# Performance work log

Measured on AMD Instinct MI355X. Metric: run time of the kernel, lower is better.

Reference implementation:

```python
import jax, jax.numpy as jnp
import numpy as np

N_HEAD, D_K, D_MODEL = 8, 64, 512  # factorized_k == d_k == d_v forced by view()/einsum consistency
B, LQ, LK = 4, 2048, 2048
TEMP = float(np.sqrt(D_K))
NEG = -1000000000.0


def setup_inputs() -> dict:
    key = jax.random.key(0)
    ks = jax.random.split(key, 8)
    q = jax.random.normal(ks[0], (B, LQ, D_MODEL), jnp.float32)
    k = jax.random.normal(ks[1], (B, LK, D_MODEL), jnp.float32)
    v = jax.random.normal(ks[2], (B, LK, D_MODEL), jnp.float32)
    mask = jax.random.randint(ks[3], (B, LQ, LK), 0, 2).astype(jnp.int32)
    # torch.rand-style positive uniform params, scaled to keep the 4-matmul chain O(1)
    W_A = jax.random.uniform(ks[4], (D_MODEL, D_K), jnp.float32, 0.0, 1.0 / D_K)
    W_A2 = jax.random.uniform(ks[5], (D_MODEL, D_K), jnp.float32, 0.0, 1.0 / D_K)
    W_A3 = jax.random.uniform(ks[6], (D_MODEL, D_K), jnp.float32, 0.0, 1.0 / D_K)
    fc_w = jax.random.normal(ks[7], (D_MODEL, N_HEAD * D_K), jnp.float32) / np.float32(np.sqrt(N_HEAD * D_K))
    ln_gamma = jnp.ones((D_MODEL,), jnp.float32)
    ln_beta = jnp.zeros((D_MODEL,), jnp.float32)
    return dict(q=q, k=k, v=v, mask=mask, W_A=W_A, W_A2=W_A2, W_A3=W_A3,
                fc_w=fc_w, ln_gamma=ln_gamma, ln_beta=ln_beta)


def reference(q, k, v, mask, W_A, W_A2, W_A3, fc_w, ln_gamma, ln_beta):
    b, lq, dm = q.shape
    lk = k.shape[1]
    residual = q
    # Since factorized_k == d_k, view(n_head,d_k,-1) and view(n_head,-1,d_k) coincide.
    W_a = W_A.reshape(N_HEAD, D_K, D_K)    # plays both 'bcd' (W_A) and 'bdi' (W_B)
    W_a2 = W_A2.reshape(N_HEAD, D_K, D_K)  # plays both 'bim' (W_At) and 'bmj' (W_Bt)
    W_av = W_A3.reshape(N_HEAD, D_K, D_K)  # plays both 'bna' (W_av) and 'bac' (W_bv)

    kt = jnp.swapaxes(k, 1, 2).reshape(b, N_HEAD, D_K, lk)  # [b,h,dk,lk]
    qh = q.reshape(b, lq, N_HEAD, D_K)                       # [b,lq,h,dk]
    vh = v.reshape(b, lk, N_HEAD, D_K)                       # [b,lk,h,dk]

    # Fold the tiny per-head weight chain first (same math as the 6-tensor einsum).
    Wq = jnp.einsum('hcd,hdi,him,hmj->hcj', W_a, W_a, W_a2, W_a2)  # [h,dk,dk]
    attn = jnp.einsum('kahc,hcj,khjn->khan', qh, Wq, kt) / TEMP     # [b,h,lq,lk]
    attn = jnp.where(mask[:, None, :, :] != 0, attn, NEG)
    attn = jax.nn.softmax(attn, axis=-1)  # dropout is identity in eval

    Wv = jnp.einsum('hna,hac->hnc', W_av, W_av)                    # [h,dk,dk]
    out = jnp.einsum('khjm,kmhn,hnc->khjc', attn, vh, Wv)          # [b,h,lq,dk]
    out = jnp.swapaxes(out, 1, 2).reshape(b, lq, N_HEAD * D_K)
    out = out @ fc_w.T  # Linear bias=False; dropout identity
    out = out + residual
    mu = jnp.mean(out, axis=-1, keepdims=True)
    var = jnp.mean((out - mu) ** 2, axis=-1, keepdims=True)
    out = (out - mu) / jnp.sqrt(var + 1e-6) * ln_gamma + ln_beta
    return (out, attn)
```

## Files before the change

### kernel.cpp

```cpp
#include <hip/hip_runtime.h>

#define B_ 4
#define H_ 8
#define L_ 2048
#define DM 512
#define DK 64

typedef __bf16 bf16x8 __attribute__((ext_vector_type(8)));
typedef float f32x4 __attribute__((ext_vector_type(4)));

__device__ __forceinline__ f32x4 mfma16(bf16x8 a, bf16x8 b, f32x4 c) {
  return __builtin_amdgcn_mfma_f32_16x16x32_bf16(a, b, c, 0, 0, 0);
}
__device__ __forceinline__ unsigned short f2bf(float f) {
  unsigned int u = __float_as_uint(f);
  u += 0x7fffu + ((u >> 16) & 1u);
  return (unsigned short)(u >> 16);
}
__device__ __forceinline__ void async16(const void* g, void* l) {
  __builtin_amdgcn_global_load_lds((const __attribute__((address_space(1))) unsigned int*)g,
                                   (__attribute__((address_space(3))) unsigned int*)l, 16, 0, 0);
}
__device__ __forceinline__ float rsum16(float v) {
  v += __shfl_xor(v, 1);
  v += __shfl_xor(v, 2);
  v += __shfl_xor(v, 4);
  v += __shfl_xor(v, 8);
  return v;
}

__device__ __forceinline__ void mm64(const float* X, const float* Y, float acc[4][4], int tr, int tc) {
#pragma unroll
  for (int rr = 0; rr < 4; ++rr)
#pragma unroll
    for (int cc = 0; cc < 4; ++cc) acc[rr][cc] = 0.f;
  for (int c = 0; c < 64; ++c) {
    float a0 = X[(tr + 0) * 65 + c], a1 = X[(tr + 1) * 65 + c];
    float a2 = X[(tr + 2) * 65 + c], a3 = X[(tr + 3) * 65 + c];
    float b0 = Y[c * 65 + tc + 0], b1 = Y[c * 65 + tc + 1];
    float b2 = Y[c * 65 + tc + 2], b3 = Y[c * 65 + tc + 3];
    acc[0][0] += a0 * b0; acc[0][1] += a0 * b1; acc[0][2] += a0 * b2; acc[0][3] += a0 * b3;
    acc[1][0] += a1 * b0; acc[1][1] += a1 * b1; acc[1][2] += a1 * b2; acc[1][3] += a1 * b3;
    acc[2][0] += a2 * b0; acc[2][1] += a2 * b1; acc[2][2] += a2 * b2; acc[2][3] += a2 * b3;
    acc[3][0] += a3 * b0; acc[3][1] += a3 * b1; acc[3][2] += a3 * b2; acc[3][3] += a3 * b3;
  }
}

__global__ __launch_bounds__(256) void k_weights(const float* __restrict__ WA, const float* __restrict__ WA2,
                                                 const float* __restrict__ WA3, float* __restrict__ Wq,
                                                 float* __restrict__ Wv) {
  __shared__ float sA[64 * 65], sB[64 * 65], sT[64 * 65];
  const int h = blockIdx.x, t = threadIdx.x;
  const int tr = (t >> 4) * 4, tc = (t & 15) * 4;
  for (int i = t; i < 4096; i += 256) {
    int r = i >> 6, c = i & 63;
    sA[r * 65 + c] = WA[h * 4096 + i];
    sB[r * 65 + c] = WA2[h * 4096 + i];
  }
  __syncthreads();
  float acc[4][4];
  mm64(sA, sA, acc, tr, tc);
#pragma unroll
  for (int rr = 0; rr < 4; ++rr)
#pragma unroll
    for (int cc = 0; cc < 4; ++cc) sT[(tr + rr) * 65 + tc + cc] = acc[rr][cc];
  __syncthreads();
  mm64(sT, sB, acc, tr, tc);
#pragma unroll
  for (int rr = 0; rr < 4; ++rr)
#pragma unroll
    for (int cc = 0; cc < 4; ++cc) sA[(tr + rr) * 65 + tc + cc] = acc[rr][cc];
  __syncthreads();
  mm64(sA, sB, acc, tr, tc);
#pragma unroll
  for (int rr = 0; rr < 4; ++rr)
#pragma unroll
    for (int cc = 0; cc < 4; ++cc) Wq[h * 4096 + (tr + rr) * 64 + tc + cc] = acc[rr][cc];
  for (int i = t; i < 4096; i += 256) {
    int r = i >> 6, c = i & 63;
    sT[r * 65 + c] = WA3[h * 4096 + i];
  }
  __syncthreads();
  mm64(sT, sT, acc, tr, tc);
#pragma unroll
  for (int rr = 0; rr < 4; ++rr)
#pragma unroll
    for (int cc = 0; cc < 4; ++cc) Wv[h * 4096 + (tr + rr) * 64 + tc + cc] = acc[rr][cc];
}

__global__ void k_conv(const float* __restrict__ s, unsigned short* __restrict__ d, int n4) {
  int i = blockIdx.x * blockDim.x + threadIdx.x;
  int stride = gridDim.x * blockDim.x;
  for (; i < n4; i += stride) {
    float4 f = ((const float4*)s)[i];
    ushort4 o;
    o.x = f2bf(f.x); o.y = f2bf(f.y); o.z = f2bf(f.z); o.w = f2bf(f.w);
    ((ushort4*)d)[i] = o;
  }
}

__global__ __launch_bounds__(256) void k_maskpack(const int* __restrict__ mask,
                                                  unsigned long long* __restrict__ mp) {
  const int row = blockIdx.x * 4 + (threadIdx.x >> 6);
  const int lane = threadIdx.x & 63;
  const int* src = mask + (size_t)row * L_;
#pragma unroll
  for (int c = 0; c < 32; ++c) {
    int mv = src[c * 64 + lane];
    unsigned long long bits = __ballot(mv != 0);
    if (lane == 0) mp[(size_t)row * 32 + c] = bits;
  }
}

__global__ __launch_bounds__(256) void k_qprime(const float* __restrict__ q, const float* __restrict__ Wq,
                                                unsigned short* __restrict__ Qp) {
  __shared__ float sW[64 * 65], sQ[64 * 65];
  const int bid = blockIdx.x;
  const int rt = bid & 31, h = (bid >> 5) & 7, b = bid >> 8;
  const int t = threadIdx.x;
  const int row0 = rt * 64;
  const float QS = 0.125f * 1.44269504088896f;
  for (int i = t; i < 4096; i += 256) {
    int r = i >> 6, c = i & 63;
    sW[r * 65 + c] = Wq[h * 4096 + i];
    sQ[r * 65 + c] = q[(size_t)(b * L_ + row0 + r) * DM + h * DK + c];
  }
  __syncthreads();
  float acc[4][4];
  const int tr = (t >> 4) * 4, tc = (t & 15) * 4;
  mm64(sQ, sW, acc, tr, tc);
#pragma unroll
  for (int rr = 0; rr < 4; ++rr) {
    ushort4 o;
    o.x = f2bf(acc[rr][0] * QS); o.y = f2bf(acc[rr][1] * QS);
    o.z = f2bf(acc[rr][2] * QS); o.w = f2bf(acc[rr][3] * QS);
    *(ushort4*)&Qp[(size_t)(b * L_ + row0 + tr + rr) * DM + h * DK + tc] = o;
  }
}

__global__ __launch_bounds__(256) void k_vprime(const float* __restrict__ v, const float* __restrict__ Wv,
                                                unsigned short* __restrict__ VpT) {
  __shared__ float sW[64 * 65], sV[64 * 65];
  __shared__ __align__(16) unsigned short ldsT[64 * 72];
  const int bid = blockIdx.x;
  const int rt = bid & 31, h = (bid >> 5) & 7, b = bid >> 8;
  const int t = threadIdx.x;
  const int key0 = rt * 64;
  for (int i = t; i < 4096; i += 256) {
    int r = i >> 6, c = i & 63;
    sW[r * 65 + c] = Wv[h * 4096 + i];
    sV[r * 65 + c] = v[(size_t)(b * L_ + key0 + r) * DM + h * DK + c];
  }
  __syncthreads();
  float acc[4][4];
  const int tr = (t >> 4) * 4, tc = (t & 15) * 4;
  mm64(sV, sW, acc, tr, tc);
#pragma unroll
  for (int rr = 0; rr < 4; ++rr)
#pragma unroll
    for (int cc = 0; cc < 4; ++cc) ldsT[(tc + cc) * 72 + tr + rr] = f2bf(acc[rr][cc]);
  __syncthreads();
  const int dk = t >> 2, kc = t & 3;
  const uint4* srcp = (const uint4*)&ldsT[dk * 72 + kc * 16];
  uint4 v0 = srcp[0], v1 = srcp[1];
  size_t go = ((size_t)((b * H_ + h) * DK + dk)) * L_ + key0 + kc * 16;
  *(uint4*)&VpT[go] = v0;
  *(uint4*)&VpT[go + 8] = v1;
}

__global__ __launch_bounds__(256) void k_attn(const unsigned short* __restrict__ Qp,
                                              const unsigned short* __restrict__ Kb,
                                              const unsigned short* __restrict__ VpT,
                                              const unsigned long long* __restrict__ mp,
                                              float* __restrict__ attn,
                                              float* __restrict__ ov) {
  __shared__ __align__(16) unsigned short KT[2][4096];
  __shared__ __align__(16) unsigned short VT[2][4096];
  __shared__ __align__(16) unsigned short PB[4][16 * 76];
  const int bid0 = blockIdx.x;
  const int bid = (bid0 & 7) * 128 + (bid0 >> 3);
  const int qt = bid & 31;
  const int h = (bid >> 5) & 7;
  const int b = bid >> 8;
  const int tid = threadIdx.x;
  const int lane = tid & 63;
  const int w = tid >> 6;
  const int l15 = lane & 15, l4 = lane >> 4;
  const int row0 = qt * 64 + w * 16;

  const unsigned short* qb = Qp + ((size_t)(b * L_ + row0 + l15)) * DM + h * DK + l4 * 8;
  const bf16x8 aQ0 = *(const bf16x8*)qb;
  const bf16x8 aQ1 = *(const bf16x8*)(qb + 32);

  const size_t kb_base = (size_t)b * L_ * DM + h * DK;
  const size_t vt_base = (size_t)((b * H_ + h) * DK) * L_;
  const unsigned long long* mrow = mp + (size_t)(b * L_ + row0 + l4 * 4) * 32;

  const int p_lo = tid * 16;
  const int skey = p_lo >> 7;
  const int sboff = (p_lo & 127) ^ ((skey & 7) << 4);
  const int skey1 = (p_lo + 4096) >> 7;
  const int sboff1 = ((p_lo + 4096) & 127) ^ ((skey1 & 7) << 4);

#define STAGE_K(kt_, s_)                                                                   \
  {                                                                                        \
    async16(Kb + kb_base + (size_t)((kt_) * 64 + skey) * DM + (sboff >> 1),                \
            (char*)&KT[s_][0] + p_lo);                                                     \
    async16(Kb + kb_base + (size_t)((kt_) * 64 + skey1) * DM + (sboff1 >> 1),              \
            (char*)&KT[s_][0] + p_lo + 4096);                                              \
  }
#define STAGE_V(kt_, s_)                                                                   \
  {                                                                                        \
    async16(VpT + vt_base + (size_t)skey * L_ + (kt_) * 64 + (sboff >> 1),                 \
            (char*)&VT[s_][0] + p_lo);                                                     \
    async16(VpT + vt_base + (size_t)skey1 * L_ + (kt_) * 64 + (sboff1 >> 1),               \
            (char*)&VT[s_][0] + p_lo + 4096);                                              \
  }

  unsigned long long mwA[4], mwB[4];
  float lsum[4] = {0.f, 0.f, 0.f, 0.f};

#pragma unroll
  for (int r = 0; r < 4; ++r) { mwA[r] = mrow[r * 32 + 0]; mwB[r] = mrow[r * 32 + 1]; }
  STAGE_K(0, 0);
  asm volatile("s_waitcnt vmcnt(0)" ::: "memory");
  __builtin_amdgcn_s_barrier();

#define P1_BODY(KT_, VMN_, DO_STAGE_, DO_LOADM_)                                           \
  {                                                                                        \
    const int kt = (KT_);                                                                  \
    const int cur = kt & 1;                                                                \
    __builtin_amdgcn_sched_barrier(0);                                                     \
    unsigned long long mwN[4] = {0ull, 0ull, 0ull, 0ull};                                  \
    if (DO_LOADM_) {                                                                       \
      _Pragma("unroll") for (int r = 0; r < 4; ++r) mwN[r] = mrow[r * 32 + kt + 2];        \
    }                                                                                      \
    if (DO_STAGE_) STAGE_K(kt + 1, cur ^ 1);                                               \
    asm volatile("s_waitcnt vmcnt(" #VMN_ ")" ::: "memory");                               \
    __builtin_amdgcn_sched_barrier(0);                                                     \
    __builtin_amdgcn_s_barrier();                                                          \
    const char* Kbase = (const char*)&KT[cur][0];                                          \
    _Pragma("unroll") for (int f = 0; f < 4; ++f) {                                        \
      int keyrow = f * 16 + l15;                                                           \
      int sw = (keyrow & 7) << 4;                                                          \
      bf16x8 b0 = *(const bf16x8*)(Kbase + keyrow * 128 + ((l4 * 16) ^ sw));               \
      bf16x8 b1 = *(const bf16x8*)(Kbase + keyrow * 128 + ((64 + l4 * 16) ^ sw));          \
      f32x4 acc = {0.f, 0.f, 0.f, 0.f};                                                    \
      acc = mfma16(aQ0, b0, acc);                                                          \
      acc = mfma16(aQ1, b1, acc);                                                          \
      _Pragma("unroll") for (int r = 0; r < 4; ++r) {                                      \
        unsigned int hb = (unsigned int)(mwA[r] >> (f * 16));                              \
        lsum[r] += ((hb >> l15) & 1u) ? exp2f(acc[r]) : 0.f;                               \
      }                                                                                    \
    }                                                                                      \
    __builtin_amdgcn_s_barrier();                                                          \
    _Pragma("unroll") for (int r = 0; r < 4; ++r) { mwA[r] = mwB[r]; mwB[r] = mwN[r]; }    \
  }

  for (int t = 0; t < 30; ++t) P1_BODY(t, 6, true, true);
  P1_BODY(30, 2, true, false);
  P1_BODY(31, 0, false, false);
#undef P1_BODY

  float invl[4];
#pragma unroll
  for (int r = 0; r < 4; ++r) invl[r] = 1.0f / rsum16(lsum[r]);

  f32x4 O[4];
#pragma unroll
  for (int d = 0; d < 4; ++d) { f32x4 z = {0.f, 0.f, 0.f, 0.f}; O[d] = z; }

  float* arow0 = attn + ((size_t)((b * H_ + h) * L_) + row0 + l4 * 4) * L_;

#pragma unroll
  for (int r = 0; r < 4; ++r) { mwA[r] = mrow[r * 32 + 0]; mwB[r] = mrow[r * 32 + 1]; }
  STAGE_K(0, 0);
  STAGE_V(0, 0);
  asm volatile("s_waitcnt vmcnt(0)" ::: "memory");
  __builtin_amdgcn_s_barrier();

#define P2_BODY(KT_, VMN_, DO_STAGE_, DO_LOADM_)                                           \
  {                                                                                        \
    const int kt = (KT_);                                                                  \
    const int cur = kt & 1;                                                                \
    const int key0 = kt * 64;                                                              \
    __builtin_amdgcn_sched_barrier(0);                                                     \
    unsigned long long mwN[4] = {0ull, 0ull, 0ull, 0ull};                                  \
    if (DO_LOADM_) {                                                                       \
      _Pragma("unroll") for (int r = 0; r < 4; ++r) mwN[r] = mrow[r * 32 + kt + 2];        \
    }                                                                                      \
    if (DO_STAGE_) { STAGE_K(kt + 1, cur ^ 1); STAGE_V(kt + 1, cur ^ 1); }                 \
    asm volatile("s_waitcnt vmcnt(" #VMN_ ")" ::: "memory");                               \
    __builtin_amdgcn_sched_barrier(0);                                                     \
    __builtin_amdgcn_s_barrier();                                                          \
    const char* Kbase = (const char*)&KT[cur][0];                                          \
    const char* Vbase = (const char*)&VT[cur][0];                                          \
    float pvv[4][4];                                                                       \
    _Pragma("unroll") for (int f = 0; f < 4; ++f) {                                        \
      int keyrow = f * 16 + l15;                                                           \
      int sw = (keyrow & 7) << 4;                                                          \
      bf16x8 b0 = *(const bf16x8*)(Kbase + keyrow * 128 + ((l4 * 16) ^ sw));               \
      bf16x8 b1 = *(const bf16x8*)(Kbase + keyrow * 128 + ((64 + l4 * 16) ^ sw));          \
      f32x4 acc = {0.f, 0.f, 0.f, 0.f};                                                    \
      acc = mfma16(aQ0, b0, acc);                                                          \
      acc = mfma16(aQ1, b1, acc);                                                          \
      _Pragma("unroll") for (int r = 0; r < 4; ++r) {                                      \
        unsigned int hb = (unsigned int)(mwA[r] >> (f * 16));                              \
        pvv[f][r] = ((hb >> l15) & 1u) ? exp2f(acc[r]) * invl[r] : 0.f;                    \
      }                                                                                    \
    }                                                                                      \
    _Pragma("unroll") for (int f = 0; f < 4; ++f)                                          \
      _Pragma("unroll") for (int r = 0; r < 4; ++r)                                        \
        __builtin_nontemporal_store(pvv[f][r],                                             \
            arow0 + (size_t)r * L_ + key0 + f * 16 + l15);                                 \
    _Pragma("unroll") for (int f = 0; f < 4; ++f)                                          \
      _Pragma("unroll") for (int r = 0; r < 4; ++r)                                        \
        PB[w][(l4 * 4 + r) * 76 + f * 16 + l15] = f2bf(pvv[f][r]);                         \
    bf16x8 aP0 = *(const bf16x8*)((const char*)&PB[w][0] + l15 * 152 + l4 * 16);           \
    bf16x8 aP1 = *(const bf16x8*)((const char*)&PB[w][0] + l15 * 152 + 64 + l4 * 16);      \
    __builtin_amdgcn_s_setprio(1);                                                         \
    _Pragma("unroll") for (int d = 0; d < 4; ++d) {                                        \
      int dkrow = d * 16 + l15;                                                            \
      int sw = (dkrow & 7) << 4;                                                           \
      bf16x8 v0 = *(const bf16x8*)(Vbase + dkrow * 128 + ((l4 * 16) ^ sw));                \
      bf16x8 v1 = *(const bf16x8*)(Vbase + dkrow * 128 + ((64 + l4 * 16) ^ sw));           \
      O[d] = mfma16(aP0, v0, O[d]);                                                        \
      O[d] = mfma16(aP1, v1, O[d]);                                                        \
    }                                                                                      \
    __builtin_amdgcn_s_setprio(0);                                                         \
    __builtin_amdgcn_s_barrier();                                                          \
    _Pragma("unroll") for (int r = 0; r < 4; ++r) { mwA[r] = mwB[r]; mwB[r] = mwN[r]; }    \
  }

  for (int t = 0; t < 30; ++t) P2_BODY(t, 24, true, true);
  P2_BODY(30, 20, true, false);
  P2_BODY(31, 16, false, false);
#undef P2_BODY

#pragma unroll
  for (int d = 0; d < 4; ++d)
#pragma unroll
    for (int r = 0; r < 4; ++r)
      ov[(size_t)(b * L_ + row0 + l4 * 4 + r) * DM + h * DK + d * 16 + l15] = O[d][r];
#undef STAGE_K
#undef STAGE_V
}

__global__ __launch_bounds__(256) void k_proj(const float* __restrict__ qres,
                                              const unsigned short* __restrict__ fcb,
                                              const float* __restrict__ gamma,
                                              const float* __restrict__ beta,
                                              float* __restrict__ io) {
  __shared__ float red1[16][4], red2[16][4];
  const int blk = blockIdx.x;
  const int tid = threadIdx.x, lane = tid & 63, w = tid >> 6;
  const int l15 = lane & 15, l4 = lane >> 4;
  const int row0 = blk * 16;
  const float* arow = io + (size_t)(row0 + l15) * DM + l4 * 8;
  const unsigned short* bb = fcb + (size_t)(w * 128 + l15) * DM + l4 * 8;
  f32x4 C[8];
#pragma unroll
  for (int i = 0; i < 8; ++i) { f32x4 z = {0.f, 0.f, 0.f, 0.f}; C[i] = z; }
  for (int kc = 0; kc < 16; ++kc) {
    float4 a0 = *(const float4*)(arow + kc * 32);
    float4 a1 = *(const float4*)(arow + kc * 32 + 4);
    union { unsigned short u[8]; bf16x8 v; } t;
    t.u[0] = f2bf(a0.x); t.u[1] = f2bf(a0.y); t.u[2] = f2bf(a0.z); t.u[3] = f2bf(a0.w);
    t.u[4] = f2bf(a1.x); t.u[5] = f2bf(a1.y); t.u[6] = f2bf(a1.z); t.u[7] = f2bf(a1.w);
#pragma unroll
    for (int cf = 0; cf < 8; ++cf) {
      bf16x8 bv = *(const bf16x8*)(bb + (size_t)(cf * 16) * DM + kc * 32);
      C[cf] = mfma16(t.v, bv, C[cf]);
    }
  }
  float s1[4] = {0.f, 0.f, 0.f, 0.f}, s2[4] = {0.f, 0.f, 0.f, 0.f};
  const int colb = w * 128;
#pragma unroll
  for (int cf = 0; cf < 8; ++cf)
#pragma unroll
    for (int r = 0; r < 4; ++r) {
      float val = C[cf][r] + qres[(size_t)(row0 + l4 * 4 + r) * DM + colb + cf * 16 + l15];
      C[cf][r] = val;
      s1[r] += val;
      s2[r] += val * val;
    }
#pragma unroll
  for (int r = 0; r < 4; ++r) { s1[r] = rsum16(s1[r]); s2[r] = rsum16(s2[r]); }
  if (l15 == 0) {
#pragma unroll
    for (int r = 0; r < 4; ++r) { red1[l4 * 4 + r][w] = s1[r]; red2[l4 * 4 + r][w] = s2[r]; }
  }
  __syncthreads();
  float mu[4], rs[4];
#pragma unroll
  for (int r = 0; r < 4; ++r) {
    int row = l4 * 4 + r;
    float t1 = red1[row][0] + red1[row][1] + red1[row][2] + red1[row][3];
    float t2 = red2[row][0] + red2[row][1] + red2[row][2] + red2[row][3];
    float m_ = t1 * (1.0f / 512.0f);
    float var = t2 * (1.0f / 512.0f) - m_ * m_;
    mu[r] = m_;
    rs[r] = rsqrtf(var + 1e-6f);
  }
#pragma unroll
  for (int cf = 0; cf < 8; ++cf) {
    float g = gamma[colb + cf * 16 + l15];
    float be = beta[colb + cf * 16 + l15];
#pragma unroll
    for (int r = 0; r < 4; ++r)
      io[(size_t)(row0 + l4 * 4 + r) * DM + colb + cf * 16 + l15] =
          (C[cf][r] - mu[r]) * rs[r] * g + be;
  }
}

extern "C" void kernel_launch(void* const* d_in, const int* in_sizes, int n_in,
                              void* d_out, int out_size, void* d_ws, size_t ws_size,
                              hipStream_t stream) {
  (void)in_sizes; (void)n_in; (void)out_size; (void)ws_size;
  const float* q   = (const float*)d_in[0];
  const float* k   = (const float*)d_in[1];
  const float* v   = (const float*)d_in[2];
  const int* mask  = (const int*)d_in[3];
  const float* WA  = (const float*)d_in[4];
  const float* WA2 = (const float*)d_in[5];
  const float* WA3 = (const float*)d_in[6];
  const float* fcw = (const float*)d_in[7];
  const float* gam = (const float*)d_in[8];
  const float* bet = (const float*)d_in[9];
  float* out = (float*)d_out;
  float* attn = out + (size_t)B_ * L_ * DM;

  char* ws = (char*)d_ws;
  float* Wq = (float*)ws;
  float* Wv = (float*)(ws + 131072);
  unsigned short* Qp  = (unsigned short*)(ws + 262144);
  unsigned short* Kb  = (unsigned short*)(ws + 262144 + 8388608);
  unsigned short* VpT = (unsigned short*)(ws + 262144 + 2 * 8388608);
  unsigned short* FCb = (unsigned short*)(ws + 262144 + 3 * 8388608);
  unsigned long long* mp = (unsigned long long*)(ws + 262144 + 3 * 8388608 + 524288);

  k_weights<<<8, 256, 0, stream>>>(WA, WA2, WA3, Wq, Wv);
  k_conv<<<1024, 256, 0, stream>>>(k, Kb, (B_ * L_ * DM) / 4);
  k_conv<<<256, 256, 0, stream>>>(fcw, FCb, (DM * DM) / 4);
  k_maskpack<<<2048, 256, 0, stream>>>(mask, mp);
  k_qprime<<<1024, 256, 0, stream>>>(q, Wq, Qp);
  k_vprime<<<1024, 256, 0, stream>>>(v, Wv, VpT);
  k_attn<<<1024, 256, 0, stream>>>(Qp, Kb, VpT, mp, attn, out);
  k_proj<<<512, 256, 0, stream>>>(q, FCb, gam, bet, out);
}
```

Baseline: 330.2 us.

## Load K fragments directly to registers in pass 1 and swizzle P buffer

The first softmax-normalizer pass now loads K MFMA fragments straight from global memory into registers with a two-deep software pipeline, instead of staging through LDS with barriers. The change also swaps exp2f for raw v_exp_f32, replaces the padded P buffer with an XOR-swizzled 128-byte row layout, and adds an occupancy hint of 4 blocks per SM. The aim is to remove LDS staging and barrier overhead in pass 1 and cut LDS bank conflicts. The cost is higher register pressure and uncoalesced global loads in pass 1, which rely on L2 hits.

New measurement: 347.6 us. +5.3%, slower.

```diff
diff --git a/kernel.cpp b/kernel.cpp
--- a/kernel.cpp
+++ b/kernel.cpp
@@ -16,6 +16,11 @@
   unsigned int u = __float_as_uint(f);
   u += 0x7fffu + ((u >> 16) & 1u);
   return (unsigned short)(u >> 16);
+}
+__device__ __forceinline__ float fexp2(float x) {
+  float r;
+  asm("v_exp_f32 %0, %1" : "=v"(r) : "v"(x));
+  return r;
 }
 __device__ __forceinline__ void async16(const void* g, void* l) {
   __builtin_amdgcn_global_load_lds((const __attribute__((address_space(1))) unsigned int*)g,
@@ -168,15 +173,15 @@
   *(uint4*)&VpT[go + 8] = v1;
 }
 
-__global__ __launch_bounds__(256) void k_attn(const unsigned short* __restrict__ Qp,
-                                              const unsigned short* __restrict__ Kb,
-                                              const unsigned short* __restrict__ VpT,
-                                              const unsigned long long* __restrict__ mp,
-                                              float* __restrict__ attn,
-                                              float* __restrict__ ov) {
+__global__ __launch_bounds__(256, 4) void k_attn(const unsigned short* __restrict__ Qp,
+                                                 const unsigned short* __restrict__ Kb,
+                                                 const unsigned short* __restrict__ VpT,
+                                                 const unsigned long long* __restrict__ mp,
+                                                 float* __restrict__ attn,
+                                                 float* __restrict__ ov) {
   __shared__ __align__(16) unsigned short KT[2][4096];
   __shared__ __align__(16) unsigned short VT[2][4096];
-  __shared__ __align__(16) unsigned short PB[4][16 * 76];
+  __shared__ __align__(16) unsigned short PB[4][1024];
   const int bid0 = blockIdx.x;
   const int bid = (bid0 & 7) * 128 + (bid0 >> 3);
   const int qt = bid & 31;
@@ -195,6 +200,62 @@
   const size_t kb_base = (size_t)b * L_ * DM + h * DK;
   const size_t vt_base = (size_t)((b * H_ + h) * DK) * L_;
   const unsigned long long* mrow = mp + (size_t)(b * L_ + row0 + l4 * 4) * 32;
+  const unsigned short* kfrag = Kb + kb_base + (size_t)l15 * DM + l4 * 8;
+
+  float lsum[4] = {0.f, 0.f, 0.f, 0.f};
+
+  bf16x8 curF[8], nxtF[8];
+  unsigned long long mwA[4], mwN[4];
+
+#define LOADK_P1(FR, kt_)                                                                  \
+  {                                                                                        \
+    _Pragma("unroll") for (int f = 0; f < 4; ++f) {                                        \
+      const unsigned short* kp = kfrag + (size_t)((kt_) * 64 + f * 16) * DM;               \
+      FR[2 * f] = *(const bf16x8*)kp;                                                      \
+      FR[2 * f + 1] = *(const bf16x8*)(kp + 32);                                           \
+    }                                                                                      \
+  }
+#define LOADM_P1(MW, kt_)                                                                  \
+  { _Pragma("unroll") for (int r = 0; r < 4; ++r) MW[r] = mrow[r * 32 + (kt_)]; }
+#define COMP_P1(FR, MW)                                                                    \
+  {                                                                                        \
+    _Pragma("unroll") for (int f = 0; f < 4; ++f) {                                        \
+      f32x4 acc = {0.f, 0.f, 0.f, 0.f};                                                    \
+      acc = mfma16(aQ0, FR[2 * f], acc);                                                   \
+      acc = mfma16(aQ1, FR[2 * f + 1], acc);                                               \
+      _Pragma("unroll") for (int r = 0; r < 4; ++r) {                                      \
+        unsigned int hb = (unsigned int)(MW[r] >> (f * 16));                               \
+        lsum[r] += ((hb >> l15) & 1u) ? fexp2(acc[r]) : 0.f;                               \
+      }                                                                                    \
+    }                                                                                      \
+  }
+
+  LOADK_P1(curF, 0);
+  LOADM_P1(mwA, 0);
+  for (int kt2 = 0; kt2 < 16; ++kt2) {
+    const int kt = kt2 * 2;
+    LOADK_P1(nxtF, kt + 1);
+    LOADM_P1(mwN, kt + 1);
+    COMP_P1(curF, mwA);
+    if (kt2 < 15) {
+      LOADK_P1(curF, kt + 2);
+      LOADM_P1(mwA, kt + 2);
+    }
+    COMP_P1(nxtF, mwN);
+  }
+#undef LOADK_P1
+#undef LOADM_P1
+#undef COMP_P1
+
+  float invl[4];
+#pragma unroll
+  for (int r = 0; r < 4; ++r) invl[r] = 1.0f / rsum16(lsum[r]);
+
+  f32x4 O[4];
+#pragma unroll
+  for (int d = 0; d < 4; ++d) { f32x4 z = {0.f, 0.f, 0.f, 0.f}; O[d] = z; }
+
+  float* arow0 = attn + ((size_t)((b * H_ + h) * L_) + row0 + l4 * 4) * L_;
 
   const int p_lo = tid * 16;
   const int skey = p_lo >> 7;
@@ -217,67 +278,15 @@
             (char*)&VT[s_][0] + p_lo + 4096);                                              \
   }
 
-  unsigned long long mwA[4], mwB[4];
-  float lsum[4] = {0.f, 0.f, 0.f, 0.f};
-
-#pragma unroll
-  for (int r = 0; r < 4; ++r) { mwA[r] = mrow[r * 32 + 0]; mwB[r] = mrow[r * 32 + 1]; }
-  STAGE_K(0, 0);
-  asm volatile("s_waitcnt vmcnt(0)" ::: "memory");
-  __builtin_amdgcn_s_barrier();
-
-#define P1_BODY(KT_, VMN_, DO_STAGE_, DO_LOADM_)                                           \
-  {                                                                                        \
-    const int kt = (KT_);                                                                  \
-    const int cur = kt & 1;                                                                \
-    __builtin_amdgcn_sched_barrier(0);                                                     \
-    unsigned long long mwN[4] = {0ull, 0ull, 0ull, 0ull};                                  \
-    if (DO_LOADM_) {                                                                       \
-      _Pragma("unroll") for (int r = 0; r < 4; ++r) mwN[r] = mrow[r * 32 + kt + 2];        \
-    }                                                                                      \
-    if (DO_STAGE_) STAGE_K(kt + 1, cur ^ 1);                                               \
-    asm volatile("s_waitcnt vmcnt(" #VMN_ ")" ::: "memory");                               \
-    __builtin_amdgcn_sched_barrier(0);                                                     \
-    __builtin_amdgcn_s_barrier();                                                          \
-    const char* Kbase = (const char*)&KT[cur][0];                                          \
-    _Pragma("unroll") for (int f = 0; f < 4; ++f) {                                        \
-      int keyrow = f * 16 + l15;                                                           \
-      int sw = (keyrow & 7) << 4;                                                          \
-      bf16x8 b0 = *(const bf16x8*)(Kbase + keyrow * 128 + ((l4 * 16) ^ sw));               \
-      bf16x8 b1 = *(const bf16x8*)(Kbase + keyrow * 128 + ((64 + l4 * 16) ^ sw));          \
-      f32x4 acc = {0.f, 0.f, 0.f, 0.f};                                                    \
-      acc = mfma16(aQ0, b0, acc);                                                          \
-      acc = mfma16(aQ1, b1, acc);                                                          \
-      _Pragma("unroll") for (int r = 0; r < 4; ++r) {                                      \
-        unsigned int hb = (unsigned int)(mwA[r] >> (f * 16));                              \
-        lsum[r] += ((hb >> l15) & 1u) ? exp2f(acc[r]) : 0.f;                               \
-      }                                                                                    \
-    }                                                                                      \
-    __builtin_amdgcn_s_barrier();                                                          \
-    _Pragma("unroll") for (int r = 0; r < 4; ++r) { mwA[r] = mwB[r]; mwB[r] = mwN[r]; }    \
-  }
-
-  for (int t = 0; t < 30; ++t) P1_BODY(t, 6, true, true);
-  P1_BODY(30, 2, true, false);
-  P1_BODY(31, 0, false, false);
-#undef P1_BODY
-
-  float invl[4];
-#pragma unroll
-  for (int r = 0; r < 4; ++r) invl[r] = 1.0f / rsum16(lsum[r]);
-
-  f32x4 O[4];
-#pragma unroll
-  for (int d = 0; d < 4; ++d) { f32x4 z = {0.f, 0.f, 0.f, 0.f}; O[d] = z; }
-
-  float* arow0 = attn + ((size_t)((b * H_ + h) * L_) + row0 + l4 * 4) * L_;
-
+  unsigned long long mwB[4];
 #pragma unroll
   for (int r = 0; r < 4; ++r) { mwA[r] = mrow[r * 32 + 0]; mwB[r] = mrow[r * 32 + 1]; }
   STAGE_K(0, 0);
   STAGE_V(0, 0);
   asm volatile("s_waitcnt vmcnt(0)" ::: "memory");
   __builtin_amdgcn_s_barrier();
+
+  char* pbw = (char*)&PB[w][0];
 
 #define P2_BODY(KT_, VMN_, DO_STAGE_, DO_LOADM_)                                           \
   {                                                                                        \
@@ -285,9 +294,9 @@
     const int cur = kt & 1;                                                                \
     const int key0 = kt * 64;                                                              \
     __builtin_amdgcn_sched_barrier(0);                                                     \
-    unsigned long long mwN[4] = {0ull, 0ull, 0ull, 0ull};                                  \
+    unsigned long long mwN2[4] = {0ull, 0ull, 0ull, 0ull};                                 \
     if (DO_LOADM_) {                                                                       \
-      _Pragma("unroll") for (int r = 0; r < 4; ++r) mwN[r] = mrow[r * 32 + kt + 2];        \
+      _Pragma("unroll") for (int r = 0; r < 4; ++r) mwN2[r] = mrow[r * 32 + kt + 2];       \
     }                                                                                      \
     if (DO_STAGE_) { STAGE_K(kt + 1, cur ^ 1); STAGE_V(kt + 1, cur ^ 1); }                 \
     asm volatile("s_waitcnt vmcnt(" #VMN_ ")" ::: "memory");                               \
@@ -306,7 +315,7 @@
       acc = mfma16(aQ1, b1, acc);                                                          \
       _Pragma("unroll") for (int r = 0; r < 4; ++r) {                                      \
         unsigned int hb = (unsigned int)(mwA[r] >> (f * 16));                              \
-        pvv[f][r] = ((hb >> l15) & 1u) ? exp2f(acc[r]) * invl[r] : 0.f;                    \
+        pvv[f][r] = ((hb >> l15) & 1u) ? fexp2(acc[r]) * invl[r] : 0.f;                    \
       }                                                                                    \
     }                                                                                      \
     _Pragma("unroll") for (int f = 0; f < 4; ++f)                                          \
@@ -314,10 +323,14 @@
         __builtin_nontemporal_store(pvv[f][r],                                             \
             arow0 + (size_t)r * L_ + key0 + f * 16 + l15);                                 \
     _Pragma("unroll") for (int f = 0; f < 4; ++f)                                          \
-      _Pragma("unroll") for (int r = 0; r < 4; ++r)                                        \
-        PB[w][(l4 * 4 + r) * 76 + f * 16 + l15] = f2bf(pvv[f][r]);                         \
-    bf16x8 aP0 = *(const bf16x8*)((const char*)&PB[w][0] + l15 * 152 + l4 * 16);           \
-    bf16x8 aP1 = *(const bf16x8*)((const char*)&PB[w][0] + l15 * 152 + 64 + l4 * 16);      \
+      _Pragma("unroll") for (int r = 0; r < 4; ++r) {                                      \
+        int prow = l4 * 4 + r;                                                             \
+        *(unsigned short*)(pbw + prow * 128 +                                              \
+                           ((f * 32 + l15 * 2) ^ ((prow & 7) << 4))) = f2bf(pvv[f][r]);    \
+      }                                                                                    \
+    int psw = (l15 & 7) << 4;                                                              \
+    bf16x8 aP0 = *(const bf16x8*)(pbw + l15 * 128 + ((l4 * 16) ^ psw));                    \
+    bf16x8 aP1 = *(const bf16x8*)(pbw + l15 * 128 + ((64 + l4 * 16) ^ psw));               \
     __builtin_amdgcn_s_setprio(1);                                                         \
     _Pragma("unroll") for (int d = 0; d < 4; ++d) {                                        \
       int dkrow = d * 16 + l15;                                                            \
@@ -329,7 +342,7 @@
     }                                                                                      \
     __builtin_amdgcn_s_setprio(0);                                                         \
     __builtin_amdgcn_s_barrier();                                                          \
-    _Pragma("unroll") for (int r = 0; r < 4; ++r) { mwA[r] = mwB[r]; mwB[r] = mwN[r]; }    \
+    _Pragma("unroll") for (int r = 0; r < 4; ++r) { mwA[r] = mwB[r]; mwB[r] = mwN2[r]; }   \
   }
 
   for (int t = 0; t < 30; ++t) P2_BODY(t, 24, true, true);
```

## Transpose QK^T MFMA so each lane owns a query row, vectorizing attn stores

Applied to the files above, without the earlier changes.

Swaps the MFMA operand order so each lane holds four consecutive keys of a single query row instead of four rows. This reduces per-lane mask state to one 64-bit word, turns the row-sum into two cross-lane shuffles, and lets attention probabilities be written as 16-byte nontemporal vector stores instead of scalar stores. The P buffer in LDS gets a swizzled 128-byte-row layout with packed 8-byte writes. Other changes: a raw v_exp_f32 replaces exp2f, vmcnt waits are adjusted to the new load counts, and launch bounds request 4 blocks per CU. The raw exp drops denormal handling, and the extra occupancy constraint may cause register spills.

After: 319.5 us. 1.03x faster.

```diff
diff --git a/kernel.cpp b/kernel.cpp
--- a/kernel.cpp
+++ b/kernel.cpp
@@ -16,6 +16,11 @@
   unsigned int u = __float_as_uint(f);
   u += 0x7fffu + ((u >> 16) & 1u);
   return (unsigned short)(u >> 16);
+}
+__device__ __forceinline__ float fexp2(float x) {
+  float r;
+  asm("v_exp_f32 %0, %1" : "=v"(r) : "v"(x));
+  return r;
 }
 __device__ __forceinline__ void async16(const void* g, void* l) {
   __builtin_amdgcn_global_load_lds((const __attribute__((address_space(1))) unsigned int*)g,
@@ -168,15 +173,15 @@
   *(uint4*)&VpT[go + 8] = v1;
 }
 
-__global__ __launch_bounds__(256) void k_attn(const unsigned short* __restrict__ Qp,
-                                              const unsigned short* __restrict__ Kb,
-                                              const unsigned short* __restrict__ VpT,
-                                              const unsigned long long* __restrict__ mp,
-                                              float* __restrict__ attn,
-                                              float* __restrict__ ov) {
+__global__ __launch_bounds__(256, 4) void k_attn(const unsigned short* __restrict__ Qp,
+                                                 const unsigned short* __restrict__ Kb,
+                                                 const unsigned short* __restrict__ VpT,
+                                                 const unsigned long long* __restrict__ mp,
+                                                 float* __restrict__ attn,
+                                                 float* __restrict__ ov) {
   __shared__ __align__(16) unsigned short KT[2][4096];
   __shared__ __align__(16) unsigned short VT[2][4096];
-  __shared__ __align__(16) unsigned short PB[4][16 * 76];
+  __shared__ __align__(16) unsigned short PB[4][1024];
   const int bid0 = blockIdx.x;
   const int bid = (bid0 & 7) * 128 + (bid0 >> 3);
   const int qt = bid & 31;
@@ -194,7 +199,7 @@
 
   const size_t kb_base = (size_t)b * L_ * DM + h * DK;
   const size_t vt_base = (size_t)((b * H_ + h) * DK) * L_;
-  const unsigned long long* mrow = mp + (size_t)(b * L_ + row0 + l4 * 4) * 32;
+  const unsigned long long* mrowl = mp + (size_t)(b * L_ + row0 + l15) * 32;
 
   const int p_lo = tid * 16;
   const int skey = p_lo >> 7;
@@ -217,11 +222,11 @@
             (char*)&VT[s_][0] + p_lo + 4096);                                              \
   }
 
-  unsigned long long mwA[4], mwB[4];
-  float lsum[4] = {0.f, 0.f, 0.f, 0.f};
-
-#pragma unroll
-  for (int r = 0; r < 4; ++r) { mwA[r] = mrow[r * 32 + 0]; mwB[r] = mrow[r * 32 + 1]; }
+  float lsum = 0.f;
+  unsigned long long mwA, mwB;
+
+  mwA = mrowl[0];
+  mwB = mrowl[1];
   STAGE_K(0, 0);
   asm volatile("s_waitcnt vmcnt(0)" ::: "memory");
   __builtin_amdgcn_s_barrier();
@@ -231,10 +236,8 @@
     const int kt = (KT_);                                                                  \
     const int cur = kt & 1;                                                                \
     __builtin_amdgcn_sched_barrier(0);                                                     \
-    unsigned long long mwN[4] = {0ull, 0ull, 0ull, 0ull};                                  \
-    if (DO_LOADM_) {                                                                       \
-      _Pragma("unroll") for (int r = 0; r < 4; ++r) mwN[r] = mrow[r * 32 + kt + 2];        \
-    }                                                                                      \
+    unsigned long long mwN = 0ull;                                                         \
+    if (DO_LOADM_) mwN = mrowl[kt + 2];                                                    \
     if (DO_STAGE_) STAGE_K(kt + 1, cur ^ 1);                                               \
     asm volatile("s_waitcnt vmcnt(" #VMN_ ")" ::: "memory");                               \
     __builtin_amdgcn_sched_barrier(0);                                                     \
@@ -246,34 +249,35 @@
       bf16x8 b0 = *(const bf16x8*)(Kbase + keyrow * 128 + ((l4 * 16) ^ sw));               \
       bf16x8 b1 = *(const bf16x8*)(Kbase + keyrow * 128 + ((64 + l4 * 16) ^ sw));          \
       f32x4 acc = {0.f, 0.f, 0.f, 0.f};                                                    \
-      acc = mfma16(aQ0, b0, acc);                                                          \
-      acc = mfma16(aQ1, b1, acc);                                                          \
-      _Pragma("unroll") for (int r = 0; r < 4; ++r) {                                      \
-        unsigned int hb = (unsigned int)(mwA[r] >> (f * 16));                              \
-        lsum[r] += ((hb >> l15) & 1u) ? exp2f(acc[r]) : 0.f;                               \
-      }                                                                                    \
+      acc = mfma16(b0, aQ0, acc);                                                          \
+      acc = mfma16(b1, aQ1, acc);                                                          \
+      unsigned nib = (unsigned)(mwA >> (f * 16 + l4 * 4));                                 \
+      _Pragma("unroll") for (int r = 0; r < 4; ++r)                                        \
+        lsum += ((nib >> r) & 1u) ? fexp2(acc[r]) : 0.f;                                   \
     }                                                                                      \
     __builtin_amdgcn_s_barrier();                                                          \
-    _Pragma("unroll") for (int r = 0; r < 4; ++r) { mwA[r] = mwB[r]; mwB[r] = mwN[r]; }    \
-  }
-
-  for (int t = 0; t < 30; ++t) P1_BODY(t, 6, true, true);
+    mwA = mwB; mwB = mwN;                                                                  \
+  }
+
+  for (int t = 0; t < 30; ++t) P1_BODY(t, 3, true, true);
   P1_BODY(30, 2, true, false);
   P1_BODY(31, 0, false, false);
 #undef P1_BODY
 
-  float invl[4];
-#pragma unroll
-  for (int r = 0; r < 4; ++r) invl[r] = 1.0f / rsum16(lsum[r]);
+  lsum += __shfl_xor(lsum, 16);
+  lsum += __shfl_xor(lsum, 32);
+  const float invl = 1.0f / lsum;
 
   f32x4 O[4];
 #pragma unroll
   for (int d = 0; d < 4; ++d) { f32x4 z = {0.f, 0.f, 0.f, 0.f}; O[d] = z; }
 
-  float* arow0 = attn + ((size_t)((b * H_ + h) * L_) + row0 + l4 * 4) * L_;
-
-#pragma unroll
-  for (int r = 0; r < 4; ++r) { mwA[r] = mrow[r * 32 + 0]; mwB[r] = mrow[r * 32 + 1]; }
+  float* arowl = attn + ((size_t)((b * H_ + h) * L_) + row0 + l15) * L_;
+  char* pbw = (char*)&PB[w][0];
+  const int psw = (l15 & 7) << 4;
+
+  mwA = mrowl[0];
+  mwB = mrowl[1];
   STAGE_K(0, 0);
   STAGE_V(0, 0);
   asm volatile("s_waitcnt vmcnt(0)" ::: "memory");
@@ -285,10 +289,8 @@
     const int cur = kt & 1;                                                                \
     const int key0 = kt * 64;                                                              \
     __builtin_amdgcn_sched_barrier(0);                                                     \
-    unsigned long long mwN[4] = {0ull, 0ull, 0ull, 0ull};                                  \
-    if (DO_LOADM_) {                                                                       \
-      _Pragma("unroll") for (int r = 0; r < 4; ++r) mwN[r] = mrow[r * 32 + kt + 2];        \
-    }                                                                                      \
+    unsigned long long mwN = 0ull;                                                         \
+    if (DO_LOADM_) mwN = mrowl[kt + 2];                                                    \
     if (DO_STAGE_) { STAGE_K(kt + 1, cur ^ 1); STAGE_V(kt + 1, cur ^ 1); }                 \
     asm volatile("s_waitcnt vmcnt(" #VMN_ ")" ::: "memory");                               \
     __builtin_amdgcn_sched_barrier(0);                                                     \
@@ -302,22 +304,25 @@
       bf16x8 b0 = *(const bf16x8*)(Kbase + keyrow * 128 + ((l4 * 16) ^ sw));               \
       bf16x8 b1 = *(const bf16x8*)(Kbase + keyrow * 128 + ((64 + l4 * 16) ^ sw));          \
       f32x4 acc = {0.f, 0.f, 0.f, 0.f};                                                    \
-      acc = mfma16(aQ0, b0, acc);                                                          \
-      acc = mfma16(aQ1, b1, acc);                                                          \
-      _Pragma("unroll") for (int r = 0; r < 4; ++r) {                                      \
-        unsigned int hb = (unsigned int)(mwA[r] >> (f * 16));                              \
-        pvv[f][r] = ((hb >> l15) & 1u) ? exp2f(acc[r]) * invl[r] : 0.f;                    \
-      }                                                                                    \
+      acc = mfma16(b0, aQ0, acc);                                                          \
+      acc = mfma16(b1, aQ1, acc);                                                          \
+      unsigned nib = (unsigned)(mwA >> (f * 16 + l4 * 4));                                 \
+      _Pragma("unroll") for (int r = 0; r < 4; ++r)                                        \
+        pvv[f][r] = ((nib >> r) & 1u) ? fexp2(acc[r]) * invl : 0.f;                        \
     }                                                                                      \
-    _Pragma("unroll") for (int f = 0; f < 4; ++f)                                          \
-      _Pragma("unroll") for (int r = 0; r < 4; ++r)                                        \
-        __builtin_nontemporal_store(pvv[f][r],                                             \
-            arow0 + (size_t)r * L_ + key0 + f * 16 + l15);                                 \
-    _Pragma("unroll") for (int f = 0; f < 4; ++f)                                          \
-      _Pragma("unroll") for (int r = 0; r < 4; ++r)                                        \
-        PB[w][(l4 * 4 + r) * 76 + f * 16 + l15] = f2bf(pvv[f][r]);                         \
-    bf16x8 aP0 = *(const bf16x8*)((const char*)&PB[w][0] + l15 * 152 + l4 * 16);           \
-    bf16x8 aP1 = *(const bf16x8*)((const char*)&PB[w][0] + l15 * 152 + 64 + l4 * 16);      \
+    _Pragma("unroll") for (int f = 0; f < 4; ++f) {                                        \
+      f32x4 sv;                                                                            \
+      sv[0] = pvv[f][0]; sv[1] = pvv[f][1]; sv[2] = pvv[f][2]; sv[3] = pvv[f][3];          \
+      __builtin_nontemporal_store(sv, (f32x4*)(arowl + key0 + f * 16 + l4 * 4));           \
+    }                                                                                      \
+    _Pragma("unroll") for (int f = 0; f < 4; ++f) {                                        \
+      ushort4 pk;                                                                          \
+      pk.x = f2bf(pvv[f][0]); pk.y = f2bf(pvv[f][1]);                                      \
+      pk.z = f2bf(pvv[f][2]); pk.w = f2bf(pvv[f][3]);                                      \
+      *(ushort4*)(pbw + l15 * 128 + ((f * 32 + l4 * 8) ^ psw)) = pk;                       \
+    }                                                                                      \
+    bf16x8 aP0 = *(const bf16x8*)(pbw + l15 * 128 + ((l4 * 16) ^ psw));                    \
+    bf16x8 aP1 = *(const bf16x8*)(pbw + l15 * 128 + ((64 + l4 * 16) ^ psw));               \
     __builtin_amdgcn_s_setprio(1);                                                         \
     _Pragma("unroll") for (int d = 0; d < 4; ++d) {                                        \
       int dkrow = d * 16 + l15;                                                            \
@@ -329,12 +334,12 @@
     }                                                                                      \
     __builtin_amdgcn_s_setprio(0);                                                         \
     __builtin_amdgcn_s_barrier();                                                          \
-    _Pragma("unroll") for (int r = 0; r < 4; ++r) { mwA[r] = mwB[r]; mwB[r] = mwN[r]; }    \
-  }
-
-  for (int t = 0; t < 30; ++t) P2_BODY(t, 24, true, true);
-  P2_BODY(30, 20, true, false);
-  P2_BODY(31, 16, false, false);
+    mwA = mwB; mwB = mwN;                                                                  \
+  }
+
+  for (int t = 0; t < 30; ++t) P2_BODY(t, 9, true, true);
+  P2_BODY(30, 8, true, false);
+  P2_BODY(31, 4, false, false);
 #undef P2_BODY
 
 #pragma unroll
```
